# Performance work log

Measured on AMD Instinct MI355X. Metric: run time of the kernel, lower is better.

The kernel has to match this reference:

```python
import jax, jax.numpy as jnp
import numpy as np
import math

D_MODEL = 1024
N_HEADS = 16
D_HEAD = D_MODEL // N_HEADS
EPS = 1e-5


def layer_norm(x, w, b):
    mu = jnp.mean(x, axis=-1, keepdims=True)
    var = jnp.mean(jnp.square(x - mu), axis=-1, keepdims=True)
    return (x - mu) * jax.lax.rsqrt(var + EPS) * w + b


def setup_inputs() -> dict:
    key = jax.random.key(0)
    ks = jax.random.split(key, 8)
    b, n, d = 1, 4096, D_MODEL
    s = 0.02
    return {
        "x": jax.random.normal(ks[0], (b, n, d), dtype=jnp.float32),
        "ln1_w": jnp.ones((d,), jnp.float32),
        "ln1_b": jnp.zeros((d,), jnp.float32),
        "ln2_w": jnp.ones((d,), jnp.float32),
        "ln2_b": jnp.zeros((d,), jnp.float32),
        "w_qkv": jax.random.normal(ks[1], (d, 3 * d), jnp.float32) * s,  # [in, out]
        "w_o": jax.random.normal(ks[2], (d, d), jnp.float32) * s,
        "w_ff1": jax.random.normal(ks[3], (d, 4 * d), jnp.float32) * s,
        "b_ff1": jnp.zeros((4 * d,), jnp.float32),
        "w_ff2": jax.random.normal(ks[4], (4 * d, d), jnp.float32) * s,
        "b_ff2": jnp.zeros((d,), jnp.float32),
    }


def reference(x, ln1_w, ln1_b, ln2_w, ln2_b, w_qkv, w_o, w_ff1, b_ff1, w_ff2, b_ff2):
    b, n, d = x.shape
    # --- attention sub-block ---
    h = layer_norm(x, ln1_w, ln1_b)
    qkv = (h @ w_qkv).reshape(b, n, 3, N_HEADS, D_HEAD)
    q, k, v = qkv[:, :, 0], qkv[:, :, 1], qkv[:, :, 2]  # [b, n, h, dh]
    scale = 1.0 / math.sqrt(D_HEAD)
    s = jnp.einsum("bqhd,bkhd->bhqk", q, k) * scale  # materialized [b,h,n,n]
    causal = jnp.tril(jnp.ones((n, n), dtype=bool))
    s = jnp.where(causal, s, -jnp.inf)
    a = jax.nn.softmax(s, axis=-1)
    out = jnp.einsum("bhqk,bkhd->bqhd", a, v).reshape(b, n, d)
    x = x + out @ w_o
    # --- FFN sub-block ---
    h2 = layer_norm(x, ln2_w, ln2_b)
    ff = jax.nn.gelu(h2 @ w_ff1 + b_ff1, approximate=False) @ w_ff2 + b_ff2
    return x + ff
```

## Files before the change

kernel.cpp:

```cpp
#include <hip/hip_runtime.h>
#include <hip/hip_bf16.h>
#include <cstdint>
#include <cstddef>

typedef __attribute__((ext_vector_type(8))) __bf16 bf16x8;
typedef __attribute__((ext_vector_type(4))) __bf16 bf16x4;
typedef __attribute__((ext_vector_type(4))) float f32x4;
typedef __attribute__((ext_vector_type(16))) float f32x16;
typedef __attribute__((ext_vector_type(4))) unsigned int uint4v;

#define MFMA16(a, b, c) __builtin_amdgcn_mfma_f32_16x16x32_bf16(a, b, c, 0, 0, 0)
#define MFMA32(a, b, c) __builtin_amdgcn_mfma_f32_32x32x16_bf16(a, b, c, 0, 0, 0)

__device__ __forceinline__ void gload_lds16(const void* g, void* l) {
  __builtin_amdgcn_global_load_lds(
      (__attribute__((address_space(1))) uint32_t*)g,
      (__attribute__((address_space(3))) uint32_t*)l,
      16, 0, 0);
}

__device__ __forceinline__ unsigned pkbf(float a, float b) {
  unsigned short x = __builtin_bit_cast(unsigned short, (__bf16)a);
  unsigned short y = __builtin_bit_cast(unsigned short, (__bf16)b);
  return (unsigned)x | ((unsigned)y << 16);
}

__global__ __launch_bounds__(256) void transpose_all_kernel(
    const float* __restrict__ w_qkv, __bf16* __restrict__ wqkvT,
    const float* __restrict__ w_o, __bf16* __restrict__ woT,
    const float* __restrict__ w_ff1, __bf16* __restrict__ wff1T,
    const float* __restrict__ w_ff2, __bf16* __restrict__ wff2T) {
  __shared__ float tile[32][33];
  int bid = blockIdx.x;
  const float* in; __bf16* out; int K, N, bx, by;
  if (bid < 3072)      { in = w_qkv; out = wqkvT; K = 1024; N = 3072; bx = bid % 96;  by = bid / 96; }
  else if (bid < 4096) { int b = bid - 3072; in = w_o;   out = woT;   K = 1024; N = 1024; bx = b % 32;  by = b / 32; }
  else if (bid < 8192) { int b = bid - 4096; in = w_ff1; out = wff1T; K = 1024; N = 4096; bx = b % 128; by = b / 128; }
  else                 { int b = bid - 8192; in = w_ff2; out = wff2T; K = 4096; N = 1024; bx = b % 32;  by = b / 32; }
  int tx = threadIdx.x, ty = threadIdx.y;
  int gcol = bx * 32 + tx;
#pragma unroll
  for (int j = 0; j < 4; j++) {
    int grow = by * 32 + ty + j * 8;
    tile[ty + j * 8][tx] = in[(size_t)grow * N + gcol];
  }
  __syncthreads();
#pragma unroll
  for (int j = 0; j < 4; j++) {
    int n = bx * 32 + ty + j * 8;
    out[(size_t)n * K + by * 32 + tx] = (__bf16)tile[tx][ty + j * 8];
  }
}

__global__ __launch_bounds__(256) void ln_kernel(
    const float* __restrict__ x, const float* __restrict__ w,
    const float* __restrict__ b, __bf16* __restrict__ out) {
  int row = blockIdx.x;
  int t = threadIdx.x;
  const float4* xr = (const float4*)(x + (size_t)row * 1024);
  float4 v = xr[t];
  float s = v.x + v.y + v.z + v.w;
  float sq = v.x * v.x + v.y * v.y + v.z * v.z + v.w * v.w;
#pragma unroll
  for (int m = 1; m < 64; m <<= 1) {
    s += __shfl_xor(s, m);
    sq += __shfl_xor(sq, m);
  }
  __shared__ float rs[4], rq[4];
  int wid = t >> 6;
  if ((t & 63) == 0) { rs[wid] = s; rq[wid] = sq; }
  __syncthreads();
  s = rs[0] + rs[1] + rs[2] + rs[3];
  sq = rq[0] + rq[1] + rq[2] + rq[3];
  float mean = s * (1.0f / 1024.0f);
  float var = sq * (1.0f / 1024.0f) - mean * mean;
  float rstd = rsqrtf(var + 1e-5f);
  int c = t * 4;
  float4 wv = ((const float4*)w)[t];
  float4 bv = ((const float4*)b)[t];
  bf16x4 o;
  o[0] = (__bf16)((v.x - mean) * rstd * wv.x + bv.x);
  o[1] = (__bf16)((v.y - mean) * rstd * wv.y + bv.y);
  o[2] = (__bf16)((v.z - mean) * rstd * wv.z + bv.z);
  o[3] = (__bf16)((v.w - mean) * rstd * wv.w + bv.w);
  *(bf16x4*)(out + (size_t)row * 1024 + c) = o;
}

__global__ __launch_bounds__(256, 2) void gemm_splitk128_kernel(
    const __bf16* __restrict__ A, const __bf16* __restrict__ BT,
    int M, int N, int K, int kchunk, __bf16* __restrict__ P) {
  __shared__ __bf16 lsA[128 * 64];
  __shared__ __bf16 lsB[128 * 64];
  int t = threadIdx.x;
  int m0 = blockIdx.y * 128, n0 = blockIdx.x * 128;
  int kbase = blockIdx.z * kchunk;
  __bf16* pout = P + (size_t)blockIdx.z * M * N;
  int wid = t >> 6, lane = t & 63, lo = lane & 15, g = lane >> 4;
  int wr = wid >> 1, wc = wid & 1;
  f32x4 acc[4][4] = {};
  const __bf16* ag = A + (size_t)(m0 + (t >> 3)) * K + (t & 7) * 8;
  const __bf16* bg = BT + (size_t)(n0 + (t >> 3)) * K + (t & 7) * 8;
  for (int k0 = kbase; k0 < kbase + kchunk; k0 += 64) {
#pragma unroll
    for (int i = 0; i < 4; i++) {
      gload_lds16(ag + (size_t)i * 32 * K + k0, &lsA[i * 2048 + t * 8]);
      gload_lds16(bg + (size_t)i * 32 * K + k0, &lsB[i * 2048 + t * 8]);
    }
    __syncthreads();
#pragma unroll
    for (int kk = 0; kk < 2; kk++) {
      bf16x8 af[4], bfr[4];
#pragma unroll
      for (int mi = 0; mi < 4; mi++)
        af[mi] = *(const bf16x8*)&lsA[(wr * 64 + mi * 16 + lo) * 64 + kk * 32 + g * 8];
#pragma unroll
      for (int ni = 0; ni < 4; ni++)
        bfr[ni] = *(const bf16x8*)&lsB[(wc * 64 + ni * 16 + lo) * 64 + kk * 32 + g * 8];
#pragma unroll
      for (int mi = 0; mi < 4; mi++)
#pragma unroll
        for (int ni = 0; ni < 4; ni++)
          acc[mi][ni] = MFMA16(af[mi], bfr[ni], acc[mi][ni]);
    }
    __syncthreads();
  }
#pragma unroll
  for (int mi = 0; mi < 4; mi++) {
#pragma unroll
    for (int ni = 0; ni < 4; ni++) {
      int col = n0 + wc * 64 + ni * 16 + lo;
      int row0 = m0 + wr * 64 + mi * 16 + g * 4;
#pragma unroll
      for (int r = 0; r < 4; r++)
        pout[(size_t)(row0 + r) * N + col] = (__bf16)acc[mi][ni][r];
    }
  }
}

__global__ __launch_bounds__(256) void out_reduce_ln_kernel(
    const __bf16* __restrict__ p0, const __bf16* __restrict__ p1,
    const float* __restrict__ x, const float* __restrict__ w,
    const float* __restrict__ b, float* __restrict__ x2,
    __bf16* __restrict__ h) {
  int row = blockIdx.x, t = threadIdx.x;
  size_t base = (size_t)row * 1024 + t * 4;
  bf16x4 a = *(const bf16x4*)&p0[base];
  bf16x4 b4 = *(const bf16x4*)&p1[base];
  float4 xv = *(const float4*)&x[base];
  float4 v;
  v.x = xv.x + (float)a[0] + (float)b4[0];
  v.y = xv.y + (float)a[1] + (float)b4[1];
  v.z = xv.z + (float)a[2] + (float)b4[2];
  v.w = xv.w + (float)a[3] + (float)b4[3];
  *(float4*)&x2[base] = v;
  float s = v.x + v.y + v.z + v.w;
  float sq = v.x * v.x + v.y * v.y + v.z * v.z + v.w * v.w;
#pragma unroll
  for (int m = 1; m < 64; m <<= 1) {
    s += __shfl_xor(s, m);
    sq += __shfl_xor(sq, m);
  }
  __shared__ float rs[4], rq[4];
  int wid = t >> 6;
  if ((t & 63) == 0) { rs[wid] = s; rq[wid] = sq; }
  __syncthreads();
  s = rs[0] + rs[1] + rs[2] + rs[3];
  sq = rq[0] + rq[1] + rq[2] + rq[3];
  float mean = s * (1.0f / 1024.0f);
  float var = sq * (1.0f / 1024.0f) - mean * mean;
  float rstd = rsqrtf(var + 1e-5f);
  float4 wv = ((const float4*)w)[t];
  float4 bv = ((const float4*)b)[t];
  bf16x4 o;
  o[0] = (__bf16)((v.x - mean) * rstd * wv.x + bv.x);
  o[1] = (__bf16)((v.y - mean) * rstd * wv.y + bv.y);
  o[2] = (__bf16)((v.z - mean) * rstd * wv.z + bv.z);
  o[3] = (__bf16)((v.w - mean) * rstd * wv.w + bv.w);
  *(bf16x4*)&h[base] = o;
}

template <int EPI>
__global__ __launch_bounds__(512, 2) void gemm256_kernel(
    const __bf16* __restrict__ A, const __bf16* __restrict__ BT,
    int M, int N, int K, int nkc,
    const float* __restrict__ bias, __bf16* __restrict__ outb,
    __bf16* __restrict__ P0, __bf16* __restrict__ P1,
    __bf16* __restrict__ P2, __bf16* __restrict__ P3) {
  __shared__ __bf16 lsA[2][2][128 * 64];
  __shared__ __bf16 lsB[2][2][128 * 64];
  int nbx = N >> 8;
  int nwg = (M >> 8) * nbx;
  int bid = blockIdx.x;
  int swz = (bid & 7) * (nwg >> 3) + (bid >> 3);
  int m0 = (swz / nbx) << 8, n0 = (swz % nbx) << 8;
  int kc = blockIdx.y;
  int kt0 = kc * nkc;
  int t = threadIdx.x;
  int wid = t >> 6, lane = t & 63, lo = lane & 15, g = lane >> 4;
  int wm = wid >> 2, wn = wid & 3;
  int srow = t >> 3, sgrp = t & 7;

  auto stA = [&](int d, int h, int kt) {
#pragma unroll
    for (int i = 0; i < 2; i++) {
      int row = i * 64 + srow;
      int gs = (sgrp ^ (row & 7)) * 8;
      gload_lds16(A + (size_t)(m0 + h * 128 + row) * K + kt * 64 + gs,
                  &lsA[d][h][(i * 512 + t) * 8]);
    }
  };
  auto stB = [&](int d, int h, int kt) {
#pragma unroll
    for (int i = 0; i < 2; i++) {
      int row = i * 64 + srow;
      int gs = (sgrp ^ (row & 7)) * 8;
      gload_lds16(BT + (size_t)(n0 + h * 128 + row) * K + kt * 64 + gs,
                  &lsB[d][h][(i * 512 + t) * 8]);
    }
  };
  auto rdA = [&](int d, int f, int kk) -> bf16x8 {
    int row = (f & 3) * 32 + wm * 16 + lo;
    return *(const bf16x8*)&lsA[d][f >> 2][row * 64 + (((kk * 4 + g) ^ (lo & 7)) * 8)];
  };
  auto rdB = [&](int d, int ni, int kk) -> bf16x8 {
    int row = (ni & 1) * 64 + wn * 16 + lo;
    return *(const bf16x8*)&lsB[d][ni >> 1][row * 64 + (((kk * 4 + g) ^ (lo & 7)) * 8)];
  };

  f32x4 acc[8][4] = {};
  stA(0, 0, kt0); stB(0, 0, kt0); stB(0, 1, kt0); stA(0, 1, kt0);
  asm volatile("s_waitcnt vmcnt(4)" ::: "memory");
  __builtin_amdgcn_s_barrier();

  for (int ki = 0; ki < nkc; ki++) {
    int kt = kt0 + ki;
    int d = ki & 1, nx = d ^ 1;
    bool pf = (ki + 1) < nkc;
    bf16x8 fa[4][2], fb0[2][2], fb1[2][2];
#pragma unroll
    for (int f = 0; f < 4; f++) { fa[f][0] = rdA(d, f, 0); fa[f][1] = rdA(d, f, 1); }
#pragma unroll
    for (int n = 0; n < 2; n++) { fb0[n][0] = rdB(d, n, 0); fb0[n][1] = rdB(d, n, 1); }
    if (pf) { stA(nx, 0, kt + 1); stB(nx, 0, kt + 1); }
    __builtin_amdgcn_s_barrier();
    __builtin_amdgcn_s_setprio(1);
#pragma unroll
    for (int f = 0; f < 4; f++)
#pragma unroll
      for (int n = 0; n < 2; n++) {
        acc[f][n] = MFMA16(fa[f][0], fb0[n][0], acc[f][n]);
        acc[f][n] = MFMA16(fa[f][1], fb0[n][1], acc[f][n]);
      }
    __builtin_amdgcn_s_setprio(0);
    asm volatile("s_waitcnt vmcnt(6)" ::: "memory");
    __builtin_amdgcn_s_barrier();
#pragma unroll
    for (int n = 0; n < 2; n++) { fb1[n][0] = rdB(d, 2 + n, 0); fb1[n][1] = rdB(d, 2 + n, 1); }
    if (pf) stB(nx, 1, kt + 1);
    __builtin_amdgcn_s_barrier();
    __builtin_amdgcn_s_setprio(1);
#pragma unroll
    for (int f = 0; f < 4; f++)
#pragma unroll
      for (int n = 0; n < 2; n++) {
        acc[f][2 + n] = MFMA16(fa[f][0], fb1[n][0], acc[f][2 + n]);
        acc[f][2 + n] = MFMA16(fa[f][1], fb1[n][1], acc[f][2 + n]);
      }
    __builtin_amdgcn_s_setprio(0);
    asm volatile("s_waitcnt vmcnt(6)" ::: "memory");
    __builtin_amdgcn_s_barrier();
#pragma unroll
    for (int f = 0; f < 4; f++) { fa[f][0] = rdA(d, 4 + f, 0); fa[f][1] = rdA(d, 4 + f, 1); }
    if (pf) stA(nx, 1, kt + 1);
    __builtin_amdgcn_s_barrier();
    __builtin_amdgcn_s_setprio(1);
#pragma unroll
    for (int f = 0; f < 4; f++)
#pragma unroll
      for (int n = 0; n < 2; n++) {
        acc[4 + f][2 + n] = MFMA16(fa[f][0], fb1[n][0], acc[4 + f][2 + n]);
        acc[4 + f][2 + n] = MFMA16(fa[f][1], fb1[n][1], acc[4 + f][2 + n]);
      }
    __builtin_amdgcn_s_setprio(0);
    __builtin_amdgcn_s_barrier();
    __builtin_amdgcn_s_setprio(1);
#pragma unroll
    for (int f = 0; f < 4; f++)
#pragma unroll
      for (int n = 0; n < 2; n++) {
        acc[4 + f][n] = MFMA16(fa[f][0], fb0[n][0], acc[4 + f][n]);
        acc[4 + f][n] = MFMA16(fa[f][1], fb0[n][1], acc[4 + f][n]);
      }
    __builtin_amdgcn_s_setprio(0);
    asm volatile("s_waitcnt vmcnt(4)" ::: "memory");
    __builtin_amdgcn_s_barrier();
  }

  __bf16* pk = (EPI == 4) ? ((kc == 0) ? P0 : (kc == 1) ? P1 : (kc == 2) ? P2 : P3)
                          : nullptr;
#pragma unroll
  for (int f = 0; f < 8; f++) {
    int row0 = m0 + (f >> 2) * 128 + (f & 3) * 32 + wm * 16 + g * 4;
#pragma unroll
    for (int ni = 0; ni < 4; ni++) {
      int col = n0 + (ni >> 1) * 128 + (ni & 1) * 64 + wn * 16 + lo;
      if (EPI == 0) {
        int sE = col >> 10, rem = col & 1023, hh = rem >> 6, dd = rem & 63;
        if (sE < 2) {
          float qs = (sE == 0) ? 0.1803368801111204f : 1.0f;
#pragma unroll
          for (int r = 0; r < 4; r++)
            outb[((size_t)(sE * 16 + hh) * 4096 + row0 + r) * 64 + dd] =
                (__bf16)(acc[f][ni][r] * qs);
        } else {
          bf16x4 pk4;
#pragma unroll
          for (int r = 0; r < 4; r++) pk4[r] = (__bf16)acc[f][ni][r];
          *(bf16x4*)&outb[(size_t)32 * 4096 * 64 + ((size_t)(hh * 64 + dd)) * 4096 + row0] = pk4;
        }
      } else if (EPI == 2) {
        float bv = bias[col];
#pragma unroll
        for (int r = 0; r < 4; r++) {
          float vv = acc[f][ni][r] + bv;
          float gg = 0.5f * vv * (1.0f + erff(vv * 0.70710678118f));
          outb[(size_t)(row0 + r) * N + col] = (__bf16)gg;
        }
      } else {
#pragma unroll
        for (int r = 0; r < 4; r++)
          pk[(size_t)(row0 + r) * N + col] = (__bf16)acc[f][ni][r];
      }
    }
  }
}

__global__ __launch_bounds__(256) void ff2_reduce_kernel(
    const __bf16* __restrict__ p0, const __bf16* __restrict__ p1,
    const __bf16* __restrict__ p2, const __bf16* __restrict__ p3,
    const float* __restrict__ x2, const float* __restrict__ bias,
    float* __restrict__ out) {
  size_t i8 = ((size_t)blockIdx.x * 256 + threadIdx.x) * 8;
  bf16x8 a = *(const bf16x8*)&p0[i8];
  bf16x8 b = *(const bf16x8*)&p1[i8];
  bf16x8 c = *(const bf16x8*)&p2[i8];
  bf16x8 d = *(const bf16x8*)&p3[i8];
  int col = (int)(i8 & 1023);
  float4 xa = *(const float4*)&x2[i8];
  float4 xb = *(const float4*)&x2[i8 + 4];
  float4 ba = *(const float4*)&bias[col];
  float4 bb = *(const float4*)&bias[col + 4];
  float4 oa, ob;
  oa.x = xa.x + ba.x + (float)a[0] + (float)b[0] + (float)c[0] + (float)d[0];
  oa.y = xa.y + ba.y + (float)a[1] + (float)b[1] + (float)c[1] + (float)d[1];
  oa.z = xa.z + ba.z + (float)a[2] + (float)b[2] + (float)c[2] + (float)d[2];
  oa.w = xa.w + ba.w + (float)a[3] + (float)b[3] + (float)c[3] + (float)d[3];
  ob.x = xb.x + bb.x + (float)a[4] + (float)b[4] + (float)c[4] + (float)d[4];
  ob.y = xb.y + bb.y + (float)a[5] + (float)b[5] + (float)c[5] + (float)d[5];
  ob.z = xb.z + bb.z + (float)a[6] + (float)b[6] + (float)c[6] + (float)d[6];
  ob.w = xb.w + bb.w + (float)a[7] + (float)b[7] + (float)c[7] + (float)d[7];
  *(float4*)&out[i8] = oa;
  *(float4*)&out[i8 + 4] = ob;
}

__global__ __launch_bounds__(512, 4) void attn_kernel(
    const __bf16* __restrict__ Q, const __bf16* __restrict__ Kb,
    const __bf16* __restrict__ VTb, __bf16* __restrict__ O) {
  constexpr int NSEQ = 4096;
  __shared__ __bf16 lds[2][2][2][64 * 64];
  int orig = blockIdx.x;
  int xcd = orig & 7, rank = orig >> 3;
  int hv = rank >> 5;
  int hd2 = (rank >> 4) & 1;
  int itr = rank & 15;
  int head = xcd * 2 + hd2;
  int it = hv ? itr : (31 - itr);
  int t = threadIdx.x, wid = t >> 6, lane = t & 63;
  int lo = lane & 31, hi = lane >> 5;
  int qsub = wid & 3, kpar = wid >> 2;
  const __bf16* kh = Kb + (size_t)head * NSEQ * 64;
  const __bf16* vth = VTb + (size_t)head * 64 * NSEQ;
  int qlow = it * 128 + qsub * 32;
  int qrow = qlow + lo;
  const __bf16* qh = Q + (size_t)head * NSEQ * 64 + (size_t)qrow * 64;
  bf16x8 bq[4];
#pragma unroll
  for (int c = 0; c < 4; c++) bq[c] = *(const bf16x8*)(qh + c * 16 + hi * 8);

  const unsigned onesu = 0x3F803F80u;
  uint4v onev = {onesu, onesu, onesu, onesu};
  bf16x8 vones = __builtin_bit_cast(bf16x8, onev);

  f32x16 acc0 = {}, acc1 = {};
  f32x16 lacc = {};
  int srow = t >> 3;
  int sgs = ((t & 7) ^ (srow & 7)) * 8;

  int off[4];
#pragma unroll
  for (int c = 0; c < 4; c++) off[c] = lo * 64 + (((c * 2 + hi) ^ (lo & 7)) * 8);
  const __bf16* lk0 = &lds[0][kpar][0][0];
  const __bf16* lk1 = &lds[1][kpar][0][0];
  const __bf16* lv0 = &lds[0][kpar][1][0];
  const __bf16* lv1 = &lds[1][kpar][1][0];
  const __bf16* khs = kh + srow * 64 + sgs;
  const __bf16* vts = vth + (size_t)srow * NSEQ + sgs;

  auto stage_tile = [&](int d, int par, int kt) {
    gload_lds16(khs + (size_t)kt * 4096, &lds[d][par][0][t * 8]);
    gload_lds16(vts + kt * 64, &lds[d][par][1][t * 8]);
  };

  int ns = it + 1;
  int qtop = qlow + 31;
  stage_tile(0, 0, 0);
  stage_tile(0, 1, 1);
  __syncthreads();

#define ATTN_STEP(CUR)                                                         \
  {                                                                            \
    if (j + 1 < ns) {                                                          \
      stage_tile((CUR) ^ 1, 0, 2 * j + 2);                                     \
      stage_tile((CUR) ^ 1, 1, 2 * j + 3);                                     \
    }                                                                          \
    int kt = 2 * j + kpar;                                                     \
    if (kt * 64 <= qtop) {                                                     \
      const __bf16* lk = (CUR) ? lk1 : lk0;                                    \
      const __bf16* lvt = (CUR) ? lv1 : lv0;                                   \
      f32x16 s0 = {}, s1 = {};                                                 \
      __builtin_amdgcn_s_setprio(1);                                           \
      _Pragma("unroll") for (int c = 0; c < 4; c++) {                          \
        bf16x8 ka0 = *(const bf16x8*)&lk[off[c]];                              \
        bf16x8 ka1 = *(const bf16x8*)&lk[2048 + off[c]];                       \
        s0 = MFMA32(ka0, bq[c], s0);                                           \
        s1 = MFMA32(ka1, bq[c], s1);                                           \
      }                                                                        \
      __builtin_amdgcn_s_setprio(0);                                           \
      if (kt * 64 + 63 > qlow) {                                               \
        _Pragma("unroll") for (int i = 0; i < 16; i++) {                       \
          int key0 = kt * 64 + (i & 3) + 8 * (i >> 2) + 4 * hi;                \
          if (key0 > qrow) s0[i] = -3.0e38f;                                   \
          if (key0 + 32 > qrow) s1[i] = -3.0e38f;                              \
        }                                                                      \
      }                                                                        \
      _Pragma("unroll") for (int i = 0; i < 16; i++) {                         \
        s0[i] = exp2f(s0[i]);                                                  \
        s1[i] = exp2f(s1[i]);                                                  \
      }                                                                        \
      uint4v pw[4];                                                            \
      _Pragma("unroll") for (int b = 0; b < 2; b++) {                          \
        int off2 = b * 8;                                                      \
        unsigned a0 = pkbf(s0[off2 + 0], s0[off2 + 1]);                        \
        unsigned a1 = pkbf(s0[off2 + 2], s0[off2 + 3]);                        \
        unsigned b0 = pkbf(s0[off2 + 4], s0[off2 + 5]);                        \
        unsigned b1 = pkbf(s0[off2 + 6], s0[off2 + 7]);                        \
        asm("v_permlane32_swap_b32 %0, %1" : "+v"(a0), "+v"(b0));              \
        asm("v_permlane32_swap_b32 %0, %1" : "+v"(a1), "+v"(b1));              \
        pw[b][0] = a0; pw[b][1] = a1; pw[b][2] = b0; pw[b][3] = b1;            \
        unsigned c0 = pkbf(s1[off2 + 0], s1[off2 + 1]);                        \
        unsigned c1 = pkbf(s1[off2 + 2], s1[off2 + 3]);                        \
        unsigned d0 = pkbf(s1[off2 + 4], s1[off2 + 5]);                        \
        unsigned d1 = pkbf(s1[off2 + 6], s1[off2 + 7]);                        \
        asm("v_permlane32_swap_b32 %0, %1" : "+v"(c0), "+v"(d0));              \
        asm("v_permlane32_swap_b32 %0, %1" : "+v"(c1), "+v"(d1));              \
        pw[2 + b][0] = c0; pw[2 + b][1] = c1; pw[2 + b][2] = d0;               \
        pw[2 + b][3] = d1;                                                     \
      }                                                                        \
      __builtin_amdgcn_s_setprio(1);                                           \
      _Pragma("unroll") for (int b = 0; b < 4; b++) {                          \
        bf16x8 pf = __builtin_bit_cast(bf16x8, pw[b]);                         \
        bf16x8 va0 = *(const bf16x8*)&lvt[off[b]];                             \
        bf16x8 va1 = *(const bf16x8*)&lvt[2048 + off[b]];                      \
        acc0 = MFMA32(va0, pf, acc0);                                          \
        acc1 = MFMA32(va1, pf, acc1);                                          \
        lacc = MFMA32(vones, pf, lacc);                                        \
      }                                                                        \
      __builtin_amdgcn_s_setprio(0);                                           \
    }                                                                          \
    __syncthreads();                                                           \
  }

  int j = 0;
  for (;;) {
    ATTN_STEP(0);
    if (++j >= ns) break;
    ATTN_STEP(1);
    if (++j >= ns) break;
  }
#undef ATTN_STEP

  float* fl = (float*)lds;
  float* lbuf = fl;
  float* ab = fl + 256;
  __bf16* bounce = (__bf16*)(fl + 256 + 9216);
  if (kpar == 1) {
    lbuf[qsub * 64 + lane] = lacc[0];
    int base = (qsub * 64 + lane) * 36;
#pragma unroll
    for (int k2 = 0; k2 < 16; k2 += 4) {
      float4 v0; v0.x = acc0[k2]; v0.y = acc0[k2 + 1]; v0.z = acc0[k2 + 2]; v0.w = acc0[k2 + 3];
      *(float4*)&ab[base + k2] = v0;
      float4 v1; v1.x = acc1[k2]; v1.y = acc1[k2 + 1]; v1.z = acc1[k2 + 2]; v1.w = acc1[k2 + 3];
      *(float4*)&ab[base + 16 + k2] = v1;
    }
  }
  __syncthreads();
  if (kpar == 0) {
    float lsum = lacc[0] + lbuf[qsub * 64 + lane];
    float linv = 1.0f / lsum;
    int base = (qsub * 64 + lane) * 36;
    f32x16 b0, b1;
#pragma unroll
    for (int k2 = 0; k2 < 16; k2 += 4) {
      float4 v0 = *(float4*)&ab[base + k2];
      b0[k2] = v0.x; b0[k2 + 1] = v0.y; b0[k2 + 2] = v0.z; b0[k2 + 3] = v0.w;
      float4 v1 = *(float4*)&ab[base + 16 + k2];
      b1[k2] = v1.x; b1[k2 + 1] = v1.y; b1[k2 + 2] = v1.z; b1[k2 + 3] = v1.w;
    }
    __bf16* region = bounce + qsub * 2048;
#pragma unroll
    for (int dt = 0; dt < 2; dt++) {
#pragma unroll
      for (int rp = 0; rp < 8; rp++) {
        int r = rp * 2;
        float a0 = dt ? acc1[r] : acc0[r], a1 = dt ? acc1[r + 1] : acc0[r + 1];
        float c0 = dt ? b1[r] : b0[r], c1 = dt ? b1[r + 1] : b0[r + 1];
        float e0 = (a0 + c0) * linv;
        float e1 = (a1 + c1) * linv;
        int d = dt * 32 + (r & 3) + 8 * (r >> 2) + 4 * hi;
        int bytecol = d * 2;
        int g16 = bytecol >> 4, rem16 = bytecol & 15;
        *(unsigned*)((char*)region + lo * 128 + ((g16 ^ (lo & 7)) * 16 + rem16)) = pkbf(e0, e1);
      }
    }
#pragma unroll
    for (int j2 = 0; j2 < 4; j2++) {
      int idx = j2 * 64 + lane;
      int row = idx >> 3, g = idx & 7;
      bf16x8 v = *(const bf16x8*)((char*)region + row * 128 + ((g ^ (row & 7)) * 16));
      *(bf16x8*)&O[(size_t)(it * 128 + qsub * 32 + row) * 1024 + head * 64 + g * 8] = v;
    }
  }
}

extern "C" void kernel_launch(void* const* d_in, const int* in_sizes, int n_in,
                              void* d_out, int out_size, void* d_ws, size_t ws_size,
                              hipStream_t stream) {
  const float* x = (const float*)d_in[0];
  const float* ln1_w = (const float*)d_in[1];
  const float* ln1_b = (const float*)d_in[2];
  const float* ln2_w = (const float*)d_in[3];
  const float* ln2_b = (const float*)d_in[4];
  const float* w_qkv = (const float*)d_in[5];
  const float* w_o = (const float*)d_in[6];
  const float* w_ff1 = (const float*)d_in[7];
  const float* b_ff1 = (const float*)d_in[8];
  const float* w_ff2 = (const float*)d_in[9];
  const float* b_ff2 = (const float*)d_in[10];
  float* out = (float*)d_out;

  const size_t D = 1024, NT = 4096;
  __bf16* wqkvT = (__bf16*)d_ws;
  __bf16* woT = wqkvT + 3072 * D;
  __bf16* wff1T = woT + D * D;
  __bf16* wff2T = wff1T + 4096 * D;
  __bf16* hbuf = wff2T + D * 4096;
  __bf16* qkvb = hbuf + NT * D;
  __bf16* attnb = qkvb + 3 * NT * D;
  __bf16* a1 = qkvb;
  float* x2 = (float*)(attnb + NT * D);
  __bf16* p0 = (__bf16*)d_ws;
  __bf16* p1 = p0 + NT * D;
  __bf16* p2 = hbuf;
  __bf16* p3 = (__bf16*)(x2 + NT * D);
  __bf16* pA = qkvb;
  __bf16* pB = pA + NT * D;

  dim3 tb(32, 8);
  transpose_all_kernel<<<12288, tb, 0, stream>>>(w_qkv, wqkvT, w_o, woT,
                                                 w_ff1, wff1T, w_ff2, wff2T);

  ln_kernel<<<4096, 256, 0, stream>>>(x, ln1_w, ln1_b, hbuf);
  gemm256_kernel<0><<<192, 512, 0, stream>>>(hbuf, wqkvT, 4096, 3072, 1024, 16,
                                             nullptr, qkvb, nullptr, nullptr, nullptr, nullptr);
  attn_kernel<<<512, 512, 0, stream>>>(
      qkvb, qkvb + 16 * NT * 64, qkvb + 32 * NT * 64, attnb);
  gemm_splitk128_kernel<<<dim3(8, 32, 2), 256, 0, stream>>>(
      attnb, woT, 4096, 1024, 1024, 512, pA);
  out_reduce_ln_kernel<<<4096, 256, 0, stream>>>(pA, pB, x, ln2_w, ln2_b, x2, hbuf);
  gemm256_kernel<2><<<256, 512, 0, stream>>>(hbuf, wff1T, 4096, 4096, 1024, 16,
                                             b_ff1, a1, nullptr, nullptr, nullptr, nullptr);
  gemm256_kernel<4><<<dim3(64, 4), 512, 0, stream>>>(a1, wff2T, 4096, 1024, 4096, 16,
                                                     nullptr, nullptr, p0, p1, p2, p3);
  ff2_reduce_kernel<<<2048, 256, 0, stream>>>(p0, p1, p2, p3, x2, b_ff2, out);
}
```

Measured before the change: 243.9 us.

## Overlap weight transposes with attention and fuse LN1 into QKV weight prep

The LN1 kernel is merged with the QKV weight transpose into a single pre-kernel launch. The remaining weight transposes (w_o, ff1, ff2) are appended as extra blocks to the attention kernel so they fill idle CUs during the causal attention tail. exp2f is also replaced by a raw v_exp_f32 instruction. The trade-offs are 512-thread transpose blocks that reserve the attention kernel's large LDS allocation and may contend with attention blocks for bandwidth, plus loss of exp2f's denormal handling.

```diff
diff --git a/kernel.cpp b/kernel.cpp
--- a/kernel.cpp
+++ b/kernel.cpp
@@ -25,38 +25,37 @@
   return (unsigned)x | ((unsigned)y << 16);
 }
 
-__global__ __launch_bounds__(256) void transpose_all_kernel(
+__device__ __forceinline__ float fexp2(float x) {
+  float r;
+  asm("v_exp_f32 %0, %1" : "=v"(r) : "v"(x));
+  return r;
+}
+
+__global__ __launch_bounds__(256) void pre_kernel(
     const float* __restrict__ w_qkv, __bf16* __restrict__ wqkvT,
-    const float* __restrict__ w_o, __bf16* __restrict__ woT,
-    const float* __restrict__ w_ff1, __bf16* __restrict__ wff1T,
-    const float* __restrict__ w_ff2, __bf16* __restrict__ wff2T) {
-  __shared__ float tile[32][33];
+    const float* __restrict__ x, const float* __restrict__ ln1_w,
+    const float* __restrict__ ln1_b, __bf16* __restrict__ h) {
+  __shared__ float sm[32 * 33];
   int bid = blockIdx.x;
-  const float* in; __bf16* out; int K, N, bx, by;
-  if (bid < 3072)      { in = w_qkv; out = wqkvT; K = 1024; N = 3072; bx = bid % 96;  by = bid / 96; }
-  else if (bid < 4096) { int b = bid - 3072; in = w_o;   out = woT;   K = 1024; N = 1024; bx = b % 32;  by = b / 32; }
-  else if (bid < 8192) { int b = bid - 4096; in = w_ff1; out = wff1T; K = 1024; N = 4096; bx = b % 128; by = b / 128; }
-  else                 { int b = bid - 8192; in = w_ff2; out = wff2T; K = 4096; N = 1024; bx = b % 32;  by = b / 32; }
   int tx = threadIdx.x, ty = threadIdx.y;
-  int gcol = bx * 32 + tx;
-#pragma unroll
-  for (int j = 0; j < 4; j++) {
-    int grow = by * 32 + ty + j * 8;
-    tile[ty + j * 8][tx] = in[(size_t)grow * N + gcol];
-  }
-  __syncthreads();
-#pragma unroll
-  for (int j = 0; j < 4; j++) {
-    int n = bx * 32 + ty + j * 8;
-    out[(size_t)n * K + by * 32 + tx] = (__bf16)tile[tx][ty + j * 8];
-  }
-}
-
-__global__ __launch_bounds__(256) void ln_kernel(
-    const float* __restrict__ x, const float* __restrict__ w,
-    const float* __restrict__ b, __bf16* __restrict__ out) {
-  int row = blockIdx.x;
-  int t = threadIdx.x;
+  if (bid < 3072) {
+    int bx = bid % 96, by = bid / 96;
+    int gcol = bx * 32 + tx;
+#pragma unroll
+    for (int j = 0; j < 4; j++) {
+      int grow = by * 32 + ty + j * 8;
+      sm[(ty + j * 8) * 33 + tx] = w_qkv[(size_t)grow * 3072 + gcol];
+    }
+    __syncthreads();
+#pragma unroll
+    for (int j = 0; j < 4; j++) {
+      int n = bx * 32 + ty + j * 8;
+      wqkvT[(size_t)n * 1024 + by * 32 + tx] = (__bf16)sm[tx * 33 + ty + j * 8];
+    }
+    return;
+  }
+  int row = bid - 3072;
+  int t = ty * 32 + tx;
   const float4* xr = (const float4*)(x + (size_t)row * 1024);
   float4 v = xr[t];
   float s = v.x + v.y + v.z + v.w;
@@ -66,7 +65,8 @@
     s += __shfl_xor(s, m);
     sq += __shfl_xor(sq, m);
   }
-  __shared__ float rs[4], rq[4];
+  float* rs = sm;
+  float* rq = sm + 4;
   int wid = t >> 6;
   if ((t & 63) == 0) { rs[wid] = s; rq[wid] = sq; }
   __syncthreads();
@@ -75,15 +75,14 @@
   float mean = s * (1.0f / 1024.0f);
   float var = sq * (1.0f / 1024.0f) - mean * mean;
   float rstd = rsqrtf(var + 1e-5f);
-  int c = t * 4;
-  float4 wv = ((const float4*)w)[t];
-  float4 bv = ((const float4*)b)[t];
+  float4 wv = ((const float4*)ln1_w)[t];
+  float4 bv = ((const float4*)ln1_b)[t];
   bf16x4 o;
   o[0] = (__bf16)((v.x - mean) * rstd * wv.x + bv.x);
   o[1] = (__bf16)((v.y - mean) * rstd * wv.y + bv.y);
   o[2] = (__bf16)((v.z - mean) * rstd * wv.z + bv.z);
   o[3] = (__bf16)((v.w - mean) * rstd * wv.w + bv.w);
-  *(bf16x4*)(out + (size_t)row * 1024 + c) = o;
+  *(bf16x4*)(h + (size_t)row * 1024 + t * 4) = o;
 }
 
 __global__ __launch_bounds__(256, 2) void gemm_splitk128_kernel(
@@ -363,19 +362,46 @@
   *(float4*)&out[i8 + 4] = ob;
 }
 
-__global__ __launch_bounds__(512, 4) void attn_kernel(
+__global__ __launch_bounds__(512, 4) void attn_fused_kernel(
     const __bf16* __restrict__ Q, const __bf16* __restrict__ Kb,
-    const __bf16* __restrict__ VTb, __bf16* __restrict__ O) {
+    const __bf16* __restrict__ VTb, __bf16* __restrict__ O,
+    const float* __restrict__ w_o, __bf16* __restrict__ woT,
+    const float* __restrict__ w_ff1, __bf16* __restrict__ wff1T,
+    const float* __restrict__ w_ff2, __bf16* __restrict__ wff2T) {
   constexpr int NSEQ = 4096;
   __shared__ __bf16 lds[2][2][2][64 * 64];
   int orig = blockIdx.x;
+  int t = threadIdx.x;
+
+  if (orig >= 512) {
+    int b = orig - 512;
+    const float* in; __bf16* outw; int K, N, bx, by;
+    if (b < 1024)      { in = w_o;   outw = woT;   K = 1024; N = 1024; bx = b & 31;  by = b >> 5; }
+    else if (b < 5120) { int c = b - 1024; in = w_ff1; outw = wff1T; K = 1024; N = 4096; bx = c & 127; by = c >> 7; }
+    else               { int c = b - 5120; in = w_ff2; outw = wff2T; K = 4096; N = 1024; bx = c & 31;  by = c >> 5; }
+    float* tile = (float*)lds;
+    int tx = t & 31, ty = t >> 5;
+#pragma unroll
+    for (int j = 0; j < 2; j++) {
+      int r = ty + j * 16;
+      tile[r * 33 + tx] = in[(size_t)(by * 32 + r) * N + bx * 32 + tx];
+    }
+    __syncthreads();
+#pragma unroll
+    for (int j = 0; j < 2; j++) {
+      int r = ty + j * 16;
+      outw[(size_t)(bx * 32 + r) * K + by * 32 + tx] = (__bf16)tile[tx * 33 + r];
+    }
+    return;
+  }
+
   int xcd = orig & 7, rank = orig >> 3;
   int hv = rank >> 5;
   int hd2 = (rank >> 4) & 1;
   int itr = rank & 15;
   int head = xcd * 2 + hd2;
   int it = hv ? itr : (31 - itr);
-  int t = threadIdx.x, wid = t >> 6, lane = t & 63;
+  int wid = t >> 6, lane = t & 63;
   int lo = lane & 31, hi = lane >> 5;
   int qsub = wid & 3, kpar = wid >> 2;
   const __bf16* kh = Kb + (size_t)head * NSEQ * 64;
@@ -444,8 +470,8 @@
         }                                                                      \
       }                                                                        \
       _Pragma("unroll") for (int i = 0; i < 16; i++) {                         \
-        s0[i] = exp2f(s0[i]);                                                  \
-        s1[i] = exp2f(s1[i]);                                                  \
+        s0[i] = fexp2(s0[i]);                                                  \
+        s1[i] = fexp2(s1[i]);                                                  \
       }                                                                        \
       uint4v pw[4];                                                            \
       _Pragma("unroll") for (int b = 0; b < 2; b++) {                          \
@@ -577,14 +603,12 @@
   __bf16* pB = pA + NT * D;
 
   dim3 tb(32, 8);
-  transpose_all_kernel<<<12288, tb, 0, stream>>>(w_qkv, wqkvT, w_o, woT,
-                                                 w_ff1, wff1T, w_ff2, wff2T);
-
-  ln_kernel<<<4096, 256, 0, stream>>>(x, ln1_w, ln1_b, hbuf);
+  pre_kernel<<<3072 + 4096, tb, 0, stream>>>(w_qkv, wqkvT, x, ln1_w, ln1_b, hbuf);
   gemm256_kernel<0><<<192, 512, 0, stream>>>(hbuf, wqkvT, 4096, 3072, 1024, 16,
                                              nullptr, qkvb, nullptr, nullptr, nullptr, nullptr);
-  attn_kernel<<<512, 512, 0, stream>>>(
-      qkvb, qkvb + 16 * NT * 64, qkvb + 32 * NT * 64, attnb);
+  attn_fused_kernel<<<512 + 9216, 512, 0, stream>>>(
+      qkvb, qkvb + 16 * NT * 64, qkvb + 32 * NT * 64, attnb,
+      w_o, woT, w_ff1, wff1T, w_ff2, wff2T);
   gemm_splitk128_kernel<<<dim3(8, 32, 2), 256, 0, stream>>>(
       attnb, woT, 4096, 1024, 1024, 512, pA);
   out_reduce_ln_kernel<<<4096, 256, 0, stream>>>(pA, pB, x, ln2_w, ln2_b, x2, hbuf);
```

Result: faster. 228.2 us (median of 2 runs) (-6.5%).
